# Performance work log

Hardware: AMD Instinct MI355X
Metric: run time of the kernel (lower is better)

## Reference

```python
import jax, jax.numpy as jnp
import numpy as np
import math

B, S, H, NH = 2, 2048, 1024, 16
DK = H // NH


def setup_inputs() -> dict:
    key = jax.random.key(0)
    k1, k2, k3 = jax.random.split(key, 3)
    scale = 1.0 / math.sqrt(H)
    return {
        "x": jax.random.normal(k1, (B, S, H), dtype=jnp.float32),
        "w_attn": jax.random.normal(k2, (H, 3 * H), dtype=jnp.float32) * scale,
        "b_attn": jnp.zeros((3 * H,), dtype=jnp.float32),
        "w_proj": jax.random.normal(k3, (H, H), dtype=jnp.float32) * scale,
        "b_proj": jnp.zeros((H,), dtype=jnp.float32),
    }


def reference(x, w_attn, b_attn, w_proj, b_proj):
    bs, seq_len, hidden = x.shape
    qkv = x @ w_attn + b_attn                       # [B,S,3H]
    q, k, v = jnp.split(qkv, 3, axis=-1)
    # [B,S,H] -> [B,NH,S,DK]
    def heads(t):
        return t.reshape(bs, seq_len, NH, DK).transpose(0, 2, 1, 3)
    q, k, v = heads(q), heads(k), heads(v)
    scores = jnp.einsum('bhqd,bhkd->bhqk', q, k) / math.sqrt(DK)  # [B,NH,S,S]
    causal = jnp.tril(jnp.ones((seq_len, seq_len), dtype=bool))
    scores = jnp.where(causal[None, None], scores, -jnp.inf)
    attn = jax.nn.softmax(scores, axis=-1)
    out = jnp.einsum('bhqk,bhkd->bhqd', attn, v)    # [B,NH,S,DK]
    out = out.transpose(0, 2, 1, 3).reshape(bs, seq_len, hidden)
    return out @ w_proj + b_proj
```

## Files before the change

### kernel.cpp

```cpp
#include <hip/hip_runtime.h>

#define BATCH 2
#define S_LEN 2048
#define NHEADS 16
#define DKV 64
#define HID 1024

typedef __attribute__((ext_vector_type(8))) short s16x8;
typedef __attribute__((ext_vector_type(4))) short s16x4;
typedef __attribute__((ext_vector_type(4))) float f32x4;

__device__ inline unsigned short f2bf(float f) {
    union { float f; unsigned int u; } v; v.f = f;
    unsigned int r = v.u + 0x7fffu + ((v.u >> 16) & 1u);
    return (unsigned short)(r >> 16);
}

__device__ inline s16x8 pack8(float4 a, float4 b) {
    s16x8 r;
    r[0] = (short)f2bf(a.x); r[1] = (short)f2bf(a.y);
    r[2] = (short)f2bf(a.z); r[3] = (short)f2bf(a.w);
    r[4] = (short)f2bf(b.x); r[5] = (short)f2bf(b.y);
    r[6] = (short)f2bf(b.z); r[7] = (short)f2bf(b.w);
    return r;
}

__device__ inline void gload_lds16(const void* g, void* l) {
    __builtin_amdgcn_global_load_lds(
        (const __attribute__((address_space(1))) void*)g,
        (__attribute__((address_space(3))) void*)l, 16, 0, 0);
}

__device__ inline unsigned int cvtpk_bf16(float lo, float hi) {
    unsigned int d;
    asm("v_cvt_pk_bf16_f32 %0, %1, %2" : "=v"(d) : "v"(lo), "v"(hi));
    return d;
}

__global__ __launch_bounds__(256)
void f32_to_bf16_kernel(const float* __restrict__ in, unsigned short* __restrict__ out, int n8) {
    int i = blockIdx.x * 256 + threadIdx.x;
    if (i < n8) {
        const float4* p = (const float4*)(in + (size_t)i * 8);
        float4 a = p[0], b = p[1];
        *(s16x8*)(out + (size_t)i * 8) = pack8(a, b);
    }
}

__global__ __launch_bounds__(256)
void transpose_bf16_kernel(const float* __restrict__ in, unsigned short* __restrict__ out,
                           int K, int N) {
    __shared__ float tile[32][33];
    int n0 = blockIdx.x * 32;
    int k0 = blockIdx.y * 32;
    int tx = threadIdx.x, ty = threadIdx.y;
    for (int i = ty; i < 32; i += 8)
        tile[i][tx] = in[(size_t)(k0 + i) * N + n0 + tx];
    __syncthreads();
    for (int i = ty; i < 32; i += 8)
        out[(size_t)(n0 + i) * K + k0 + tx] = f2bf(tile[tx][i]);
}

__global__ __launch_bounds__(256)
void gemm_qkv_kernel(const unsigned short* __restrict__ A, const unsigned short* __restrict__ Bt,
                     const float* __restrict__ bias, unsigned short* __restrict__ qkv,
                     unsigned short* __restrict__ vT, int M, int N, int K) {
    __shared__ __align__(16) unsigned short As[2][128 * 32];
    __shared__ __align__(16) unsigned short Bs[2][128 * 32];

    const int tid  = threadIdx.x;
    const int lane = tid & 63;
    const int wv   = tid >> 6;
    const int wr   = wv >> 1, wc = wv & 1;
    const int m0   = blockIdx.y * 128, n0 = blockIdx.x * 128;

    const int lr = lane & 15;
    const int lg = lane >> 4;
    const int lk = lg * 8;

    const int srow = lane >> 2;
    const int scol = (lane & 3) * 8;

    f32x4 acc[4][4] = {};
    int cur = 0;

    #pragma unroll
    for (int l = 0; l < 2; l++) {
        const int r0 = wv * 32 + l * 16;
        gload_lds16(A  + (size_t)(m0 + r0 + srow) * K + scol, &As[0][r0 * 32]);
        gload_lds16(Bt + (size_t)(n0 + r0 + srow) * K + scol, &Bs[0][r0 * 32]);
    }

    for (int k0 = 0; k0 < K; k0 += 32) {
        __syncthreads();

        if (k0 + 32 < K) {
            #pragma unroll
            for (int l = 0; l < 2; l++) {
                const int r0 = wv * 32 + l * 16;
                gload_lds16(A  + (size_t)(m0 + r0 + srow) * K + k0 + 32 + scol, &As[cur ^ 1][r0 * 32]);
                gload_lds16(Bt + (size_t)(n0 + r0 + srow) * K + k0 + 32 + scol, &Bs[cur ^ 1][r0 * 32]);
            }
        }

        s16x8 af[4], bfr[4];
        #pragma unroll
        for (int mi = 0; mi < 4; mi++)
            af[mi] = *(const s16x8*)&As[cur][(wr * 64 + mi * 16 + lr) * 32 + lk];
        #pragma unroll
        for (int ni = 0; ni < 4; ni++)
            bfr[ni] = *(const s16x8*)&Bs[cur][(wc * 64 + ni * 16 + lr) * 32 + lk];
        #pragma unroll
        for (int mi = 0; mi < 4; mi++)
            #pragma unroll
            for (int ni = 0; ni < 4; ni++)
                acc[mi][ni] = __builtin_amdgcn_mfma_f32_16x16x32_bf16(af[mi], bfr[ni], acc[mi][ni], 0, 0, 0);
        cur ^= 1;
    }

    const bool isV = (n0 >= 2 * HID);
    #pragma unroll
    for (int mi = 0; mi < 4; mi++) {
        #pragma unroll
        for (int ni = 0; ni < 4; ni++) {
            int col = n0 + wc * 64 + ni * 16 + lr;
            float bv = bias[col];
            int row0 = m0 + wr * 64 + mi * 16 + lg * 4;
            if (isV) {
                int d = col - 2 * HID;
                int bb = row0 >> 11;
                int s = row0 & (S_LEN - 1);
                int sl = s & 63;
                int sp = (sl & 0x23) | ((sl & 0x10) >> 2) | ((sl & 0x0C) << 1);
                int sc = (s & ~63) | sp;
                s16x4 pk;
                #pragma unroll
                for (int r = 0; r < 4; r++)
                    pk[r] = (short)f2bf(acc[mi][ni][r] + bv);
                *(s16x4*)&vT[((size_t)bb * HID + d) * S_LEN + sc] = pk;
            } else {
                #pragma unroll
                for (int r = 0; r < 4; r++)
                    qkv[(size_t)(row0 + r) * N + col] = f2bf(acc[mi][ni][r] + bv);
            }
        }
    }
}

__global__ __launch_bounds__(256)
void gemm64_kernel(const unsigned short* __restrict__ A, const unsigned short* __restrict__ Bt,
                   const float* __restrict__ bias, float* __restrict__ Cout,
                   int M, int N, int K) {
    __shared__ __align__(16) unsigned short As[2][64 * 32];
    __shared__ __align__(16) unsigned short Bs[2][128 * 32];

    const int tid  = threadIdx.x;
    const int lane = tid & 63;
    const int wv   = tid >> 6;
    const int wr   = wv >> 1, wc = wv & 1;
    const int m0   = blockIdx.y * 64, n0 = blockIdx.x * 128;

    const int lr = lane & 15;
    const int lg = lane >> 4;
    const int lk = lg * 8;

    const int srow = lane >> 2;
    const int scol = (lane & 3) * 8;

    const int arow = tid >> 2;
    const int acol = (tid & 3) * 8;

    f32x4 acc[2][4] = {};
    int cur = 0;

    gload_lds16(A + (size_t)(m0 + arow) * K + acol, &As[0][(arow & ~3) * 32]);
    #pragma unroll
    for (int l = 0; l < 2; l++) {
        const int r0 = wv * 32 + l * 16;
        gload_lds16(Bt + (size_t)(n0 + r0 + srow) * K + scol, &Bs[0][r0 * 32]);
    }

    for (int k0 = 0; k0 < K; k0 += 32) {
        __syncthreads();

        if (k0 + 32 < K) {
            gload_lds16(A + (size_t)(m0 + arow) * K + k0 + 32 + acol, &As[cur ^ 1][(arow & ~3) * 32]);
            #pragma unroll
            for (int l = 0; l < 2; l++) {
                const int r0 = wv * 32 + l * 16;
                gload_lds16(Bt + (size_t)(n0 + r0 + srow) * K + k0 + 32 + scol, &Bs[cur ^ 1][r0 * 32]);
            }
        }

        s16x8 af[2], bfr[4];
        #pragma unroll
        for (int mi = 0; mi < 2; mi++)
            af[mi] = *(const s16x8*)&As[cur][(wr * 32 + mi * 16 + lr) * 32 + lk];
        #pragma unroll
        for (int ni = 0; ni < 4; ni++)
            bfr[ni] = *(const s16x8*)&Bs[cur][(wc * 64 + ni * 16 + lr) * 32 + lk];
        #pragma unroll
        for (int mi = 0; mi < 2; mi++)
            #pragma unroll
            for (int ni = 0; ni < 4; ni++)
                acc[mi][ni] = __builtin_amdgcn_mfma_f32_16x16x32_bf16(af[mi], bfr[ni], acc[mi][ni], 0, 0, 0);
        cur ^= 1;
    }

    #pragma unroll
    for (int mi = 0; mi < 2; mi++) {
        #pragma unroll
        for (int ni = 0; ni < 4; ni++) {
            int col = n0 + wc * 64 + ni * 16 + lr;
            float bv = bias[col];
            #pragma unroll
            for (int r = 0; r < 4; r++) {
                int row = m0 + wr * 32 + mi * 16 + lg * 4 + r;
                Cout[(size_t)row * N + col] = acc[mi][ni][r] + bv;
            }
        }
    }
}

__global__ __launch_bounds__(256)
void attn_kernel(const unsigned short* __restrict__ qkv, const unsigned short* __restrict__ vT,
                 unsigned short* __restrict__ out) {
    __shared__ __align__(16) unsigned short Ks[2][64 * 64];
    __shared__ __align__(16) unsigned short Vs[2][64 * 64];

    const int tid  = threadIdx.x;
    const int lane = tid & 63;
    const int w    = tid >> 6;

    const int wgid = blockIdx.x;
    const int xcd  = wgid & 7;
    const int slot = wgid >> 3;
    const int pp   = slot & 15;
    const int g    = (slot >> 4) * 8 + xcd;
    const int head = g & 15;
    const int b    = g >> 4;

    const size_t rowbase = (size_t)b * S_LEN;
    const int hoff = head * DKV;

    const int lr = lane & 15;
    const int lg = lane >> 4;
    const int lk = lg * 8;

    const int krow   = lane >> 3;
    const int kchunk = ((lane & 7) ^ krow) * 8;

    #pragma unroll
    for (int panel = 0; panel < 2; panel++) {
        const int qb = (panel == 0) ? pp : (31 - pp);
        const int q0 = qb * 64;
        const int nt = qb + 1;

        s16x8 qf[2];
        {
            const unsigned short* qp = qkv + (rowbase + q0 + w * 16 + lr) * (3 * HID) + hoff;
            qf[0] = *(const s16x8*)(qp + lk);
            qf[1] = *(const s16x8*)(qp + 32 + lk);
        }

        f32x4 o[4] = {};
        float lsum = 0.0f;
        int cur = 0;

        __syncthreads();
        #pragma unroll
        for (int l = 0; l < 2; l++) {
            const int r0 = (w * 2 + l) * 8;
            gload_lds16(qkv + (rowbase + r0 + krow) * (3 * HID) + HID + hoff + kchunk,
                        &Ks[0][r0 * 64]);
            gload_lds16(vT + ((size_t)b * HID + hoff + r0 + krow) * S_LEN + kchunk,
                        &Vs[0][r0 * 64]);
        }

        for (int tt = 0; tt < nt; tt++) {
            __syncthreads();

            if (tt + 1 < nt) {
                const int jn = (tt + 1) * 64;
                #pragma unroll
                for (int l = 0; l < 2; l++) {
                    const int r0 = (w * 2 + l) * 8;
                    gload_lds16(qkv + (rowbase + jn + r0 + krow) * (3 * HID) + HID + hoff + kchunk,
                                &Ks[cur ^ 1][r0 * 64]);
                    gload_lds16(vT + ((size_t)b * HID + hoff + r0 + krow) * S_LEN + jn + kchunk,
                                &Vs[cur ^ 1][r0 * 64]);
                }
            }

            f32x4 sfT[4] = {};
            #pragma unroll
            for (int kt = 0; kt < 2; kt++)
                #pragma unroll
                for (int ni = 0; ni < 4; ni++) {
                    s16x8 kb = *(const s16x8*)&Ks[cur][(ni * 16 + lr) * 64 + (((kt * 4 + lg) ^ (lr & 7)) * 8)];
                    sfT[ni] = __builtin_amdgcn_mfma_f32_16x16x32_bf16(kb, qf[kt], sfT[ni], 0, 0, 0);
                }

            const bool diag = (tt == nt - 1);
            unsigned int own[4][2];
            #pragma unroll
            for (int ni = 0; ni < 4; ni++) {
                float pv[4];
                #pragma unroll
                for (int r = 0; r < 4; r++) {
                    float s = sfT[ni][r];
                    if (diag) {
                        int kl = ni * 16 + lg * 4 + r;
                        if (kl > w * 16 + lr) s = -INFINITY;
                    }
                    pv[r] = exp2f(__fmaf_rn(s, 0.18033688f, -17.3123405f));
                }
                lsum += (pv[0] + pv[1]) + (pv[2] + pv[3]);
                own[ni][0] = cvtpk_bf16(pv[0], pv[1]);
                own[ni][1] = cvtpk_bf16(pv[2], pv[3]);
            }

            #pragma unroll
            for (int kt = 0; kt < 2; kt++) {
                union { unsigned int u[4]; s16x8 v; } pa;
                pa.u[0] = own[2 * kt][0];
                pa.u[1] = own[2 * kt][1];
                pa.u[2] = own[2 * kt + 1][0];
                pa.u[3] = own[2 * kt + 1][1];
                #pragma unroll
                for (int dt = 0; dt < 4; dt++) {
                    s16x8 vb = *(const s16x8*)&Vs[cur][(dt * 16 + lr) * 64 + (((kt * 4 + lg) ^ (lr & 7)) * 8)];
                    o[dt] = __builtin_amdgcn_mfma_f32_16x16x32_bf16(vb, pa.v, o[dt], 0, 0, 0);
                }
            }
            cur ^= 1;
        }

        lsum += __shfl_xor(lsum, 16, 64);
        lsum += __shfl_xor(lsum, 32, 64);
        float invl = 1.0f / lsum;
        int qrow = q0 + w * 16 + lr;
        #pragma unroll
        for (int dt = 0; dt < 4; dt++) {
            s16x4 pk;
            #pragma unroll
            for (int r = 0; r < 4; r++) pk[r] = (short)f2bf(o[dt][r] * invl);
            *(s16x4*)&out[(rowbase + qrow) * HID + hoff + dt * 16 + lg * 4] = pk;
        }
    }
}

extern "C" void kernel_launch(void* const* d_in, const int* in_sizes, int n_in,
                              void* d_out, int out_size, void* d_ws, size_t ws_size,
                              hipStream_t stream) {
    const float* x      = (const float*)d_in[0];
    const float* w_attn = (const float*)d_in[1];
    const float* b_attn = (const float*)d_in[2];
    const float* w_proj = (const float*)d_in[3];
    const float* b_proj = (const float*)d_in[4];
    float* out = (float*)d_out;

    char* ws = (char*)d_ws;
    unsigned short* qkv      = (unsigned short*)(ws);
    unsigned short* waT      = (unsigned short*)(ws + 25165824);
    unsigned short* wpT      = (unsigned short*)(ws + 31457280);
    unsigned short* attn_out = (unsigned short*)(ws + 33554432);
    unsigned short* xb       = (unsigned short*)(ws + 41943040);
    unsigned short* vTr      = (unsigned short*)(ws + 50331648);

    const int M = BATCH * S_LEN;

    f32_to_bf16_kernel<<<dim3((M * HID / 8 + 255) / 256), 256, 0, stream>>>(x, xb, M * HID / 8);

    dim3 tb(32, 8);
    transpose_bf16_kernel<<<dim3(3 * HID / 32, HID / 32), tb, 0, stream>>>(w_attn, waT, HID, 3 * HID);
    transpose_bf16_kernel<<<dim3(HID / 32, HID / 32), tb, 0, stream>>>(w_proj, wpT, HID, HID);

    gemm_qkv_kernel<<<dim3(3 * HID / 128, M / 128), 256, 0, stream>>>(
        xb, waT, b_attn, qkv, vTr, M, 3 * HID, HID);

    attn_kernel<<<dim3(512), 256, 0, stream>>>(qkv, vTr, attn_out);

    gemm64_kernel<<<dim3(HID / 128, M / 64), 256, 0, stream>>>(
        attn_out, wpT, b_proj, out, M, HID, HID);
}
```

Measured before the change: 121.9 us.

## Split attention KV loop across two workgroups and combine partials

```diff
diff --git a/kernel.cpp b/kernel.cpp
--- a/kernel.cpp
+++ b/kernel.cpp
@@ -14,6 +14,11 @@
     union { float f; unsigned int u; } v; v.f = f;
     unsigned int r = v.u + 0x7fffu + ((v.u >> 16) & 1u);
     return (unsigned short)(r >> 16);
+}
+
+__device__ inline float bf2f(unsigned short u) {
+    union { unsigned int u; float f; } v; v.u = ((unsigned int)u) << 16;
+    return v.f;
 }
 
 __device__ inline s16x8 pack8(float4 a, float4 b) {
@@ -141,7 +146,7 @@
             } else {
                 #pragma unroll
                 for (int r = 0; r < 4; r++)
-                    qkv[(size_t)(row0 + r) * N + col] = f2bf(acc[mi][ni][r] + bv);
+                    qkv[(size_t)(row0 + r) * (2 * HID) + col] = f2bf(acc[mi][ni][r] + bv);
             }
         }
     }
@@ -224,7 +229,7 @@
 
 __global__ __launch_bounds__(256)
 void attn_kernel(const unsigned short* __restrict__ qkv, const unsigned short* __restrict__ vT,
-                 unsigned short* __restrict__ out) {
+                 unsigned short* __restrict__ partO, float* __restrict__ partL) {
     __shared__ __align__(16) unsigned short Ks[2][64 * 64];
     __shared__ __align__(16) unsigned short Vs[2][64 * 64];
 
@@ -235,8 +240,9 @@
     const int wgid = blockIdx.x;
     const int xcd  = wgid & 7;
     const int slot = wgid >> 3;
-    const int pp   = slot & 15;
-    const int g    = (slot >> 4) * 8 + xcd;
+    const int pp   = (slot & 31) >> 1;
+    const int c    = slot & 1;
+    const int g    = (slot >> 5) * 8 + xcd;
     const int head = g & 15;
     const int b    = g >> 4;
 
@@ -254,11 +260,10 @@
     for (int panel = 0; panel < 2; panel++) {
         const int qb = (panel == 0) ? pp : (31 - pp);
         const int q0 = qb * 64;
-        const int nt = qb + 1;
 
         s16x8 qf[2];
         {
-            const unsigned short* qp = qkv + (rowbase + q0 + w * 16 + lr) * (3 * HID) + hoff;
+            const unsigned short* qp = qkv + (rowbase + q0 + w * 16 + lr) * (2 * HID) + hoff;
             qf[0] = *(const s16x8*)(qp + lk);
             qf[1] = *(const s16x8*)(qp + 32 + lk);
         }
@@ -268,24 +273,27 @@
         int cur = 0;
 
         __syncthreads();
-        #pragma unroll
-        for (int l = 0; l < 2; l++) {
-            const int r0 = (w * 2 + l) * 8;
-            gload_lds16(qkv + (rowbase + r0 + krow) * (3 * HID) + HID + hoff + kchunk,
-                        &Ks[0][r0 * 64]);
-            gload_lds16(vT + ((size_t)b * HID + hoff + r0 + krow) * S_LEN + kchunk,
-                        &Vs[0][r0 * 64]);
-        }
-
-        for (int tt = 0; tt < nt; tt++) {
+        if (c <= qb) {
+            const int j0 = c * 64;
+            #pragma unroll
+            for (int l = 0; l < 2; l++) {
+                const int r0 = (w * 2 + l) * 8;
+                gload_lds16(qkv + (rowbase + j0 + r0 + krow) * (2 * HID) + HID + hoff + kchunk,
+                            &Ks[0][r0 * 64]);
+                gload_lds16(vT + ((size_t)b * HID + hoff + r0 + krow) * S_LEN + j0 + kchunk,
+                            &Vs[0][r0 * 64]);
+            }
+        }
+
+        for (int t = c; t <= qb; t += 2) {
             __syncthreads();
 
-            if (tt + 1 < nt) {
-                const int jn = (tt + 1) * 64;
+            if (t + 2 <= qb) {
+                const int jn = (t + 2) * 64;
                 #pragma unroll
                 for (int l = 0; l < 2; l++) {
                     const int r0 = (w * 2 + l) * 8;
-                    gload_lds16(qkv + (rowbase + jn + r0 + krow) * (3 * HID) + HID + hoff + kchunk,
+                    gload_lds16(qkv + (rowbase + jn + r0 + krow) * (2 * HID) + HID + hoff + kchunk,
                                 &Ks[cur ^ 1][r0 * 64]);
                     gload_lds16(vT + ((size_t)b * HID + hoff + r0 + krow) * S_LEN + jn + kchunk,
                                 &Vs[cur ^ 1][r0 * 64]);
@@ -301,7 +309,7 @@
                     sfT[ni] = __builtin_amdgcn_mfma_f32_16x16x32_bf16(kb, qf[kt], sfT[ni], 0, 0, 0);
                 }
 
-            const bool diag = (tt == nt - 1);
+            const bool diag = (t == qb);
             unsigned int own[4][2];
             #pragma unroll
             for (int ni = 0; ni < 4; ni++) {
@@ -338,16 +346,51 @@
 
         lsum += __shfl_xor(lsum, 16, 64);
         lsum += __shfl_xor(lsum, 32, 64);
-        float invl = 1.0f / lsum;
-        int qrow = q0 + w * 16 + lr;
+        const size_t pi = (size_t)(g * 32 + qb) * 2 + c;
+        const int qrow = w * 16 + lr;
         #pragma unroll
         for (int dt = 0; dt < 4; dt++) {
             s16x4 pk;
             #pragma unroll
-            for (int r = 0; r < 4; r++) pk[r] = (short)f2bf(o[dt][r] * invl);
-            *(s16x4*)&out[(rowbase + qrow) * HID + hoff + dt * 16 + lg * 4] = pk;
-        }
-    }
+            for (int r = 0; r < 4; r++) pk[r] = (short)f2bf(o[dt][r]);
+            *(s16x4*)&partO[pi * 4096 + qrow * 64 + dt * 16 + lg * 4] = pk;
+        }
+        if (lg == 0) partL[pi * 64 + qrow] = lsum;
+    }
+}
+
+__global__ __launch_bounds__(256)
+void combine_kernel(const unsigned short* __restrict__ partO, const float* __restrict__ partL,
+                    unsigned short* __restrict__ out) {
+    const int idx = blockIdx.x;
+    const int g = idx >> 5, qb = idx & 31;
+    const int head = g & 15, b = g >> 4;
+    const int tid = threadIdx.x;
+
+    const size_t p0 = (size_t)(idx * 2) * 4096;
+    const size_t p1 = p0 + 4096;
+    const int loff = idx * 2 * 64;
+
+    const int i0 = tid * 16;
+    const int q = i0 >> 6;
+    const int d0 = i0 & 63;
+    float invl = 1.0f / (partL[loff + q] + partL[loff + 64 + q]);
+
+    s16x8 a0 = *(const s16x8*)&partO[p0 + i0];
+    s16x8 a1 = *(const s16x8*)&partO[p0 + i0 + 8];
+    s16x8 b0 = *(const s16x8*)&partO[p1 + i0];
+    s16x8 b1 = *(const s16x8*)&partO[p1 + i0 + 8];
+
+    s16x8 r0, r1;
+    #pragma unroll
+    for (int j = 0; j < 8; j++) {
+        r0[j] = (short)f2bf((bf2f((unsigned short)a0[j]) + bf2f((unsigned short)b0[j])) * invl);
+        r1[j] = (short)f2bf((bf2f((unsigned short)a1[j]) + bf2f((unsigned short)b1[j])) * invl);
+    }
+
+    const size_t oaddr = ((size_t)b * S_LEN + qb * 64 + q) * HID + head * DKV + d0;
+    *(s16x8*)&out[oaddr]     = r0;
+    *(s16x8*)&out[oaddr + 8] = r1;
 }
 
 extern "C" void kernel_launch(void* const* d_in, const int* in_sizes, int n_in,
@@ -362,11 +405,13 @@
 
     char* ws = (char*)d_ws;
     unsigned short* qkv      = (unsigned short*)(ws);
-    unsigned short* waT      = (unsigned short*)(ws + 25165824);
-    unsigned short* wpT      = (unsigned short*)(ws + 31457280);
-    unsigned short* attn_out = (unsigned short*)(ws + 33554432);
-    unsigned short* xb       = (unsigned short*)(ws + 41943040);
-    unsigned short* vTr      = (unsigned short*)(ws + 50331648);
+    unsigned short* waT      = (unsigned short*)(ws + 16777216);
+    unsigned short* wpT      = (unsigned short*)(ws + 23068672);
+    unsigned short* attn_out = (unsigned short*)(ws + 25165824);
+    unsigned short* xb       = (unsigned short*)(ws + 33554432);
+    unsigned short* vTr      = (unsigned short*)(ws + 41943040);
+    unsigned short* partO    = (unsigned short*)(ws + 50331648);
+    float*          partL    = (float*)(ws + 67108864);
 
     const int M = BATCH * S_LEN;
 
@@ -379,7 +424,9 @@
     gemm_qkv_kernel<<<dim3(3 * HID / 128, M / 128), 256, 0, stream>>>(
         xb, waT, b_attn, qkv, vTr, M, 3 * HID, HID);
 
-    attn_kernel<<<dim3(512), 256, 0, stream>>>(qkv, vTr, attn_out);
+    attn_kernel<<<dim3(1024), 256, 0, stream>>>(qkv, vTr, partO, partL);
+
+    combine_kernel<<<dim3(1024), 256, 0, stream>>>(partO, partL, attn_out);
 
     gemm64_kernel<<<dim3(HID / 128, M / 64), 256, 0, stream>>>(
         attn_out, wpT, b_proj, out, M, HID, HID);
```

Result: no change. 121.7 us (-0.2%).

## Split attention KV loop across two wave groups and remap QKV GEMM tiles per XCD

Applied to the files above, without the earlier changes.

```diff
diff --git a/kernel.cpp b/kernel.cpp
--- a/kernel.cpp
+++ b/kernel.cpp
@@ -72,7 +72,12 @@
     const int lane = tid & 63;
     const int wv   = tid >> 6;
     const int wr   = wv >> 1, wc = wv & 1;
-    const int m0   = blockIdx.y * 128, n0 = blockIdx.x * 128;
+
+    const int wg  = blockIdx.x;
+    const int xcd = wg & 7;
+    const int idx = wg >> 3;
+    const int m0  = (idx & 31) * 128;
+    const int n0  = (xcd * 3 + (idx >> 5)) * 128;
 
     const int lr = lane & 15;
     const int lg = lane >> 4;
@@ -141,7 +146,7 @@
             } else {
                 #pragma unroll
                 for (int r = 0; r < 4; r++)
-                    qkv[(size_t)(row0 + r) * N + col] = f2bf(acc[mi][ni][r] + bv);
+                    qkv[(size_t)(row0 + r) * (2 * HID) + col] = f2bf(acc[mi][ni][r] + bv);
             }
         }
     }
@@ -222,15 +227,17 @@
     }
 }
 
-__global__ __launch_bounds__(256)
+__global__ __launch_bounds__(512)
 void attn_kernel(const unsigned short* __restrict__ qkv, const unsigned short* __restrict__ vT,
                  unsigned short* __restrict__ out) {
-    __shared__ __align__(16) unsigned short Ks[2][64 * 64];
-    __shared__ __align__(16) unsigned short Vs[2][64 * 64];
+    __shared__ __align__(16) unsigned short Ks[2][2][64 * 64];
+    __shared__ __align__(16) unsigned short Vs[2][2][64 * 64];
 
     const int tid  = threadIdx.x;
     const int lane = tid & 63;
-    const int w    = tid >> 6;
+    const int wv   = tid >> 6;
+    const int grp  = wv >> 2;
+    const int w    = wv & 3;
 
     const int wgid = blockIdx.x;
     const int xcd  = wgid & 7;
@@ -250,15 +257,17 @@
     const int krow   = lane >> 3;
     const int kchunk = ((lane & 7) ^ krow) * 8;
 
+    float* scratch = (float*)&Ks[0][0][0];
+
     #pragma unroll
     for (int panel = 0; panel < 2; panel++) {
         const int qb = (panel == 0) ? pp : (31 - pp);
         const int q0 = qb * 64;
-        const int nt = qb + 1;
+        const int niter = (qb + 2) >> 1;
 
         s16x8 qf[2];
         {
-            const unsigned short* qp = qkv + (rowbase + q0 + w * 16 + lr) * (3 * HID) + hoff;
+            const unsigned short* qp = qkv + (rowbase + q0 + w * 16 + lr) * (2 * HID) + hoff;
             qf[0] = *(const s16x8*)(qp + lk);
             qf[1] = *(const s16x8*)(qp + 32 + lk);
         }
@@ -268,84 +277,109 @@
         int cur = 0;
 
         __syncthreads();
-        #pragma unroll
-        for (int l = 0; l < 2; l++) {
-            const int r0 = (w * 2 + l) * 8;
-            gload_lds16(qkv + (rowbase + r0 + krow) * (3 * HID) + HID + hoff + kchunk,
-                        &Ks[0][r0 * 64]);
-            gload_lds16(vT + ((size_t)b * HID + hoff + r0 + krow) * S_LEN + kchunk,
-                        &Vs[0][r0 * 64]);
-        }
-
-        for (int tt = 0; tt < nt; tt++) {
+        if (grp <= qb) {
+            const int j0 = grp * 64;
+            #pragma unroll
+            for (int l = 0; l < 2; l++) {
+                const int r0 = (w * 2 + l) * 8;
+                gload_lds16(qkv + (rowbase + j0 + r0 + krow) * (2 * HID) + HID + hoff + kchunk,
+                            &Ks[grp][0][r0 * 64]);
+                gload_lds16(vT + ((size_t)b * HID + hoff + r0 + krow) * S_LEN + j0 + kchunk,
+                            &Vs[grp][0][r0 * 64]);
+            }
+        }
+
+        for (int it = 0; it < niter; it++) {
+            const int t = 2 * it + grp;
             __syncthreads();
 
-            if (tt + 1 < nt) {
-                const int jn = (tt + 1) * 64;
+            if (t + 2 <= qb) {
+                const int jn = (t + 2) * 64;
                 #pragma unroll
                 for (int l = 0; l < 2; l++) {
                     const int r0 = (w * 2 + l) * 8;
-                    gload_lds16(qkv + (rowbase + jn + r0 + krow) * (3 * HID) + HID + hoff + kchunk,
-                                &Ks[cur ^ 1][r0 * 64]);
+                    gload_lds16(qkv + (rowbase + jn + r0 + krow) * (2 * HID) + HID + hoff + kchunk,
+                                &Ks[grp][cur ^ 1][r0 * 64]);
                     gload_lds16(vT + ((size_t)b * HID + hoff + r0 + krow) * S_LEN + jn + kchunk,
-                                &Vs[cur ^ 1][r0 * 64]);
+                                &Vs[grp][cur ^ 1][r0 * 64]);
                 }
             }
 
-            f32x4 sfT[4] = {};
-            #pragma unroll
-            for (int kt = 0; kt < 2; kt++)
+            if (t <= qb) {
+                f32x4 sfT[4] = {};
+                #pragma unroll
+                for (int kt = 0; kt < 2; kt++)
+                    #pragma unroll
+                    for (int ni = 0; ni < 4; ni++) {
+                        s16x8 kb = *(const s16x8*)&Ks[grp][cur][(ni * 16 + lr) * 64 + (((kt * 4 + lg) ^ (lr & 7)) * 8)];
+                        sfT[ni] = __builtin_amdgcn_mfma_f32_16x16x32_bf16(kb, qf[kt], sfT[ni], 0, 0, 0);
+                    }
+
+                const bool diag = (t == qb);
+                unsigned int own[4][2];
                 #pragma unroll
                 for (int ni = 0; ni < 4; ni++) {
-                    s16x8 kb = *(const s16x8*)&Ks[cur][(ni * 16 + lr) * 64 + (((kt * 4 + lg) ^ (lr & 7)) * 8)];
-                    sfT[ni] = __builtin_amdgcn_mfma_f32_16x16x32_bf16(kb, qf[kt], sfT[ni], 0, 0, 0);
+                    float pv[4];
+                    #pragma unroll
+                    for (int r = 0; r < 4; r++) {
+                        float s = sfT[ni][r];
+                        if (diag) {
+                            int kl = ni * 16 + lg * 4 + r;
+                            if (kl > w * 16 + lr) s = -INFINITY;
+                        }
+                        pv[r] = exp2f(__fmaf_rn(s, 0.18033688f, -17.3123405f));
+                    }
+                    lsum += (pv[0] + pv[1]) + (pv[2] + pv[3]);
+                    own[ni][0] = cvtpk_bf16(pv[0], pv[1]);
+                    own[ni][1] = cvtpk_bf16(pv[2], pv[3]);
                 }
 
-            const bool diag = (tt == nt - 1);
-            unsigned int own[4][2];
-            #pragma unroll
-            for (int ni = 0; ni < 4; ni++) {
-                float pv[4];
-                #pragma unroll
-                for (int r = 0; r < 4; r++) {
-                    float s = sfT[ni][r];
-                    if (diag) {
-                        int kl = ni * 16 + lg * 4 + r;
-                        if (kl > w * 16 + lr) s = -INFINITY;
+                #pragma unroll
+                for (int kt = 0; kt < 2; kt++) {
+                    union { unsigned int u[4]; s16x8 v; } pa;
+                    pa.u[0] = own[2 * kt][0];
+                    pa.u[1] = own[2 * kt][1];
+                    pa.u[2] = own[2 * kt + 1][0];
+                    pa.u[3] = own[2 * kt + 1][1];
+                    #pragma unroll
+                    for (int dt = 0; dt < 4; dt++) {
+                        s16x8 vb = *(const s16x8*)&Vs[grp][cur][(dt * 16 + lr) * 64 + (((kt * 4 + lg) ^ (lr & 7)) * 8)];
+                        o[dt] = __builtin_amdgcn_mfma_f32_16x16x32_bf16(vb, pa.v, o[dt], 0, 0, 0);
                     }
-                    pv[r] = exp2f(__fmaf_rn(s, 0.18033688f, -17.3123405f));
                 }
-                lsum += (pv[0] + pv[1]) + (pv[2] + pv[3]);
-                own[ni][0] = cvtpk_bf16(pv[0], pv[1]);
-                own[ni][1] = cvtpk_bf16(pv[2], pv[3]);
-            }
-
-            #pragma unroll
-            for (int kt = 0; kt < 2; kt++) {
-                union { unsigned int u[4]; s16x8 v; } pa;
-                pa.u[0] = own[2 * kt][0];
-                pa.u[1] = own[2 * kt][1];
-                pa.u[2] = own[2 * kt + 1][0];
-                pa.u[3] = own[2 * kt + 1][1];
-                #pragma unroll
-                for (int dt = 0; dt < 4; dt++) {
-                    s16x8 vb = *(const s16x8*)&Vs[cur][(dt * 16 + lr) * 64 + (((kt * 4 + lg) ^ (lr & 7)) * 8)];
-                    o[dt] = __builtin_amdgcn_mfma_f32_16x16x32_bf16(vb, pa.v, o[dt], 0, 0, 0);
-                }
             }
             cur ^= 1;
         }
 
-        lsum += __shfl_xor(lsum, 16, 64);
-        lsum += __shfl_xor(lsum, 32, 64);
-        float invl = 1.0f / lsum;
-        int qrow = q0 + w * 16 + lr;
-        #pragma unroll
-        for (int dt = 0; dt < 4; dt++) {
-            s16x4 pk;
-            #pragma unroll
-            for (int r = 0; r < 4; r++) pk[r] = (short)f2bf(o[dt][r] * invl);
-            *(s16x4*)&out[(rowbase + qrow) * HID + hoff + dt * 16 + lg * 4] = pk;
+        __syncthreads();
+        const int sbase = (w * 64 + lane) * 17;
+        if (grp == 1) {
+            #pragma unroll
+            for (int dt = 0; dt < 4; dt++)
+                #pragma unroll
+                for (int r = 0; r < 4; r++)
+                    scratch[sbase + dt * 4 + r] = o[dt][r];
+            scratch[sbase + 16] = lsum;
+        }
+        __syncthreads();
+        if (grp == 0) {
+            #pragma unroll
+            for (int dt = 0; dt < 4; dt++)
+                #pragma unroll
+                for (int r = 0; r < 4; r++)
+                    o[dt][r] += scratch[sbase + dt * 4 + r];
+            lsum += scratch[sbase + 16];
+            lsum += __shfl_xor(lsum, 16, 64);
+            lsum += __shfl_xor(lsum, 32, 64);
+            float invl = 1.0f / lsum;
+            int qrow = q0 + w * 16 + lr;
+            #pragma unroll
+            for (int dt = 0; dt < 4; dt++) {
+                s16x4 pk;
+                #pragma unroll
+                for (int r = 0; r < 4; r++) pk[r] = (short)f2bf(o[dt][r] * invl);
+                *(s16x4*)&out[(rowbase + qrow) * HID + hoff + dt * 16 + lg * 4] = pk;
+            }
         }
     }
 }
@@ -362,11 +396,11 @@
 
     char* ws = (char*)d_ws;
     unsigned short* qkv      = (unsigned short*)(ws);
-    unsigned short* waT      = (unsigned short*)(ws + 25165824);
-    unsigned short* wpT      = (unsigned short*)(ws + 31457280);
-    unsigned short* attn_out = (unsigned short*)(ws + 33554432);
-    unsigned short* xb       = (unsigned short*)(ws + 41943040);
-    unsigned short* vTr      = (unsigned short*)(ws + 50331648);
+    unsigned short* waT      = (unsigned short*)(ws + 16777216);
+    unsigned short* wpT      = (unsigned short*)(ws + 23068672);
+    unsigned short* attn_out = (unsigned short*)(ws + 25165824);
+    unsigned short* xb       = (unsigned short*)(ws + 33554432);
+    unsigned short* vTr      = (unsigned short*)(ws + 41943040);
 
     const int M = BATCH * S_LEN;
 
@@ -376,10 +410,10 @@
     transpose_bf16_kernel<<<dim3(3 * HID / 32, HID / 32), tb, 0, stream>>>(w_attn, waT, HID, 3 * HID);
     transpose_bf16_kernel<<<dim3(HID / 32, HID / 32), tb, 0, stream>>>(w_proj, wpT, HID, HID);
 
-    gemm_qkv_kernel<<<dim3(3 * HID / 128, M / 128), 256, 0, stream>>>(
+    gemm_qkv_kernel<<<dim3(768), 256, 0, stream>>>(
         xb, waT, b_attn, qkv, vTr, M, 3 * HID, HID);
 
-    attn_kernel<<<dim3(512), 256, 0, stream>>>(qkv, vTr, attn_out);
+    attn_kernel<<<dim3(512), 512, 0, stream>>>(qkv, vTr, attn_out);
 
     gemm64_kernel<<<dim3(HID / 128, M / 64), 256, 0, stream>>>(
         attn_out, wpT, b_proj, out, M, HID, HID);
```

New measurement: 118.3 us. 3.0% less time.
